# Kernel optimization log

Hardware: AMD Instinct MI355X
Metric: run time of the kernel (lower is better)

## Reference

```python
import jax, jax.numpy as jnp
import numpy as np

B, N, F, H, K, HID, TAB = 4, 256, 1024, 16, 128, 4096, 32
D = F // H
PI = 3.14159  # matches literal in source


def setup_inputs() -> dict:
    key = jax.random.key(0)
    ks = jax.random.split(key, 20)
    r = lambda i, shape: jax.random.normal(ks[i], shape, jnp.float32) * 0.02
    return dict(
        nfeat=jax.random.normal(ks[0], (B, N, F), jnp.float32),
        sp_dist=jax.random.randint(ks[1], (B, N, N), 0, TAB, dtype=jnp.int32),
        rd_dist=jax.random.uniform(ks[2], (B, N, N), jnp.float32),
        dist_table=r(3, (TAB, K)),
        g_means=jax.random.uniform(ks[4], (K,), jnp.float32, 0.0, 3.0),
        g_stds=jax.random.uniform(ks[5], (K,), jnp.float32, 0.0, 3.0),
        g_mul=jnp.ones((1,), jnp.float32),
        g_bias=jnp.zeros((1,), jnp.float32),
        mlp_w1=r(6, (2 * K, H)), mlp_b1=jnp.zeros((H,), jnp.float32),
        mlp_w2=r(7, (H, H)), mlp_b2=jnp.zeros((H,), jnp.float32),
        wq=r(8, (F, F)), bq=jnp.zeros((F,), jnp.float32),
        wk=r(9, (F, F)), bk=jnp.zeros((F,), jnp.float32),
        wv=r(10, (F, F)), bv=jnp.zeros((F,), jnp.float32),
        wo=r(11, (F, F)), bo=jnp.zeros((F,), jnp.float32),
        ffn_w1=r(12, (F, HID)), ffn_b1=jnp.zeros((HID,), jnp.float32),
        ffn_w2=r(13, (HID, F)), ffn_b2=jnp.zeros((F,), jnp.float32),
        ln1_g=jnp.ones((F,), jnp.float32), ln1_b=jnp.zeros((F,), jnp.float32),
        ln2_g=jnp.ones((F,), jnp.float32), ln2_b=jnp.zeros((F,), jnp.float32),
    )


def _layer_norm(x, g, b):
    m = x.mean(-1, keepdims=True)
    v = ((x - m) ** 2).mean(-1, keepdims=True)
    return (x - m) / jnp.sqrt(v + 1e-5) * g + b


def reference(nfeat, sp_dist, rd_dist, dist_table, g_means, g_stds, g_mul, g_bias,
              mlp_w1, mlp_b1, mlp_w2, mlp_b2, wq, bq, wk, bk, wv, bv, wo, bo,
              ffn_w1, ffn_b1, ffn_w2, ffn_b2, ln1_g, ln1_b, ln2_g, ln2_b):
    # --- FusedDistEncoder: shortest-path embedding + Gaussian resistance-distance encoding ---
    sp_emb = dist_table[sp_dist]                      # [B,N,N,K]
    x = g_mul * rd_dist[..., None] + g_bias           # [B,N,N,1] -> broadcast over K
    std = jnp.abs(g_stds) + 0.01                      # [K]
    rd_emb = jnp.exp(-0.5 * ((x - g_means) / std) ** 2) / (((2 * PI) ** 0.5) * std)
    h = jnp.concatenate([sp_emb, rd_emb], axis=-1)    # [B,N,N,2K]
    h = jax.nn.gelu(h @ mlp_w1 + mlp_b1, approximate=False)
    attn_bias = h @ mlp_w2 + mlp_b2                   # [B,N,N,H]

    # --- BiasedMultiheadAttention (note: source divides q by scaling=d^-0.5, i.e. *sqrt(d)) ---
    q = (nfeat @ wq + bq).reshape(B, N, H, D) * (D ** 0.5)
    k = (nfeat @ wk + bk).reshape(B, N, H, D)
    v = (nfeat @ wv + bv).reshape(B, N, H, D)
    scores = jnp.einsum('bihd,bjhd->bijh', q, k) + attn_bias   # [B,N,N,H]
    w = jax.nn.softmax(scores, axis=2)                          # softmax over key dim j
    attn = jnp.einsum('bijh,bjhd->bihd', w, v).reshape(B, N, F) @ wo + bo

    # --- GraphormerLayer residuals (post-norm, dropout=0 / eval) ---
    x1 = _layer_norm(nfeat + attn, ln1_g, ln1_b)
    ffn = jax.nn.relu(x1 @ ffn_w1 + ffn_b1) @ ffn_w2 + ffn_b2
    return _layer_norm(x1 + ffn, ln2_g, ln2_b)
```

## Files before the change

kernel.cpp:

```cpp
#include <hip/hip_runtime.h>
#include <hip/hip_bf16.h>
#include <math.h>

typedef __hip_bfloat16 bf16;
typedef float f32x4 __attribute__((ext_vector_type(4)));
typedef short bf16x8 __attribute__((ext_vector_type(8)));

#define AS1 __attribute__((address_space(1)))
#define AS3 __attribute__((address_space(3)))

#define ASM_VMCNT4 asm volatile("s_waitcnt vmcnt(4)" ::: "memory")
#define ASM_VMCNT0 asm volatile("s_waitcnt vmcnt(0)" ::: "memory")
#define ASM_LGKM0  asm volatile("s_waitcnt lgkmcnt(0)" ::: "memory")
#define ASM_BARRIER asm volatile("s_barrier" ::: "memory")

__global__ __launch_bounds__(256) void setup_kernel(
    const float* __restrict__ nfeat, bf16* __restrict__ nfeatb,
    const float* __restrict__ bq, const float* __restrict__ bk,
    const float* __restrict__ bv, float* __restrict__ bqkv,
    const float* __restrict__ table, const float* __restrict__ w1,
    float* __restrict__ tw)
{
    int bid = blockIdx.x, t = threadIdx.x;
    if (bid < 1024) {
        int i = (bid * 256 + t) * 4;
        float4 v = *reinterpret_cast<const float4*>(nfeat + i);
        nfeatb[i + 0] = (bf16)v.x; nfeatb[i + 1] = (bf16)v.y;
        nfeatb[i + 2] = (bf16)v.z; nfeatb[i + 3] = (bf16)v.w;
    } else if (bid < 1036) {
        int i = (bid - 1024) * 256 + t;
        bqkv[i] = i < 1024 ? bq[i] : (i < 2048 ? bk[i - 1024] : bv[i - 2048]);
    } else {
        #pragma unroll
        for (int e = t; e < 512; e += 256) {
            int r = e >> 4, o = e & 15;
            float a = 0.f;
            for (int k = 0; k < 128; ++k) a += table[r * 128 + k] * w1[k * 16 + o];
            tw[e] = a;
        }
    }
}

__global__ __launch_bounds__(256) void wtx_kernel(
    const float* __restrict__ wq, const float* __restrict__ wk,
    const float* __restrict__ wv, const float* __restrict__ wo,
    const float* __restrict__ fw1, const float* __restrict__ fw2,
    bf16* __restrict__ qkvT, bf16* __restrict__ woT,
    bf16* __restrict__ fw1T, bf16* __restrict__ fw2T)
{
    __shared__ float tile[64][68];
    int bid = blockIdx.x, t = threadIdx.x;
    const float* W; bf16* WT; int Kd, Nd, local;
    if (bid < 768)       { int ws = bid >> 8; local = bid & 255;
                           W = ws == 0 ? wq : ws == 1 ? wk : wv;
                           WT = qkvT + ws * 1048576; Kd = 1024; Nd = 1024; }
    else if (bid < 1024) { local = bid - 768;  W = wo;  WT = woT;  Kd = 1024; Nd = 1024; }
    else if (bid < 2048) { local = bid - 1024; W = fw1; WT = fw1T; Kd = 1024; Nd = 4096; }
    else                 { local = bid - 2048; W = fw2; WT = fw2T; Kd = 4096; Nd = 1024; }
    int ntn = Nd >> 6;
    int k0 = (local / ntn) * 64, n0 = (local % ntn) * 64;

    {
        int k = t >> 2, nb = (t & 3) * 16;
        const float* src = W + (size_t)(k0 + k) * Nd + n0 + nb;
        #pragma unroll
        for (int c = 0; c < 4; c++) {
            float4 v = *reinterpret_cast<const float4*>(src + c * 4);
            *reinterpret_cast<float4*>(&tile[k][nb + c * 4]) = v;
        }
    }
    __syncthreads();

    {
        int w = t >> 6, l = t & 63;
        int n = w * 16 + (l >> 2), kb = (l & 3) * 16;
        bf16x8 o0, o1;
        #pragma unroll
        for (int j = 0; j < 8; j++) {
            union { bf16 b; short s; } u;
            u.b = (bf16)tile[kb + j][n];
            o0[j] = u.s;
        }
        #pragma unroll
        for (int j = 0; j < 8; j++) {
            union { bf16 b; short s; } u;
            u.b = (bf16)tile[kb + 8 + j][n];
            o1[j] = u.s;
        }
        bf16* dst = WT + (size_t)(n0 + n) * Kd + k0 + kb;
        *reinterpret_cast<bf16x8*>(dst) = o0;
        *reinterpret_cast<bf16x8*>(dst + 8) = o1;
    }
}

__global__ __launch_bounds__(256) void enc_kernel(
    const int* __restrict__ sp, const float* __restrict__ rd,
    const float* __restrict__ tw,
    const float* __restrict__ means, const float* __restrict__ stds,
    const float* __restrict__ gmul, const float* __restrict__ gbias,
    const float* __restrict__ w1, const float* __restrict__ b1,
    const float* __restrict__ w2, const float* __restrict__ b2,
    bf16* __restrict__ biasT)
{
    __shared__ float w1s[128][16];
    __shared__ float w2s[16][16];
    __shared__ float b1s[16], b2s[16];
    __shared__ float meanS[128], istdS[128], coefS[128];
    int t = threadIdx.x;
    for (int i = t; i < 2048; i += 256) w1s[i >> 4][i & 15] = w1[2048 + i];
    w2s[t >> 4][t & 15] = w2[t];
    if (t < 16) { b1s[t] = b1[t]; b2s[t] = b2[t]; }
    if (t < 128) {
        float s = fabsf(stds[t]) + 0.01f;
        meanS[t] = means[t];
        istdS[t] = 1.f / s;
        coefS[t] = 1.f / (sqrtf(2.f * 3.14159f) * s);
    }
    __syncthreads();

    int p = blockIdx.x * 256 + t;
    int idx = sp[p];
    float xv = gmul[0] * rd[p] + gbias[0];

    float acc[16];
    #pragma unroll
    for (int o = 0; o < 16; o++) acc[o] = b1s[o] + tw[idx * 16 + o];

    for (int k = 0; k < 128; k++) {
        float d = (xv - meanS[k]) * istdS[k];
        float g = coefS[k] * __expf(-0.5f * d * d);
        #pragma unroll
        for (int o = 0; o < 16; o++) acc[o] += g * w1s[k][o];
    }
    float h[16];
    #pragma unroll
    for (int o = 0; o < 16; o++) {
        float a = acc[o];
        h[o] = 0.5f * a * (1.f + erff(a * 0.70710678118f));
    }
    float outv[16];
    #pragma unroll
    for (int o = 0; o < 16; o++) outv[o] = b2s[o];
    #pragma unroll
    for (int q = 0; q < 16; q++) {
        float hq = h[q];
        #pragma unroll
        for (int o = 0; o < 16; o++) outv[o] += hq * w2s[q][o];
    }
    int b = blockIdx.x >> 8, i = blockIdx.x & 255;
    #pragma unroll
    for (int hh = 0; hh < 16; hh++)
        biasT[(((b * 16 + hh) * 256 + i) << 8) + t] = (bf16)outv[hh];
}

__global__ __launch_bounds__(256, 4) void gemm_bf16(
    const bf16* __restrict__ A, const bf16* __restrict__ BT,
    const float* __restrict__ bias, const float* __restrict__ add,
    void* __restrict__ C, int M, int Nd, int Kd, int epi)
{
    __shared__ __align__(16) char smem[32768];
    int t = threadIdx.x;
    int w = t >> 6, l = t & 63;
    int wr = w >> 1, wc = w & 1;
    int lr = l & 15, hi = l >> 4;
    int row0 = blockIdx.y * 64, col0 = blockIdx.x * 64;
    int nz = gridDim.z;
    int klen = Kd / nz;
    int kbeg = blockIdx.z * klen;

    f32x4 acc[2][2];
    #pragma unroll
    for (int i = 0; i < 2; i++)
        #pragma unroll
        for (int j = 0; j < 2; j++) acc[i][j] = (f32x4){0.f, 0.f, 0.f, 0.f};

    const bf16* Asrc = A + (row0 + (t & 63)) * Kd + kbeg + (t >> 6) * 8;
    const bf16* Bsrc = BT + (col0 + (t & 63)) * Kd + kbeg + (t >> 6) * 8;
    int wbase = (t & 192) * 16;

    #pragma unroll
    for (int p = 0; p < 2; p++) {
        __builtin_amdgcn_global_load_lds((const AS1 void*)(Asrc + p * 32),
                                         (AS3 void*)(smem + p * 4096 + wbase), 16, 0, 0);
        __builtin_amdgcn_global_load_lds((const AS1 void*)(Bsrc + p * 32),
                                         (AS3 void*)(smem + 8192 + p * 4096 + wbase), 16, 0, 0);
    }

    int nsteps = klen >> 6;
    int cur = 0;
    for (int s = 0; s < nsteps; ++s) {
        int nxt = cur ^ 1;
        if (s + 1 < nsteps) {
            const bf16* An = Asrc + (s + 1) * 64;
            const bf16* Bn = Bsrc + (s + 1) * 64;
            #pragma unroll
            for (int p = 0; p < 2; p++) {
                __builtin_amdgcn_global_load_lds((const AS1 void*)(An + p * 32),
                    (AS3 void*)(smem + nxt * 16384 + p * 4096 + wbase), 16, 0, 0);
                __builtin_amdgcn_global_load_lds((const AS1 void*)(Bn + p * 32),
                    (AS3 void*)(smem + nxt * 16384 + 8192 + p * 4096 + wbase), 16, 0, 0);
            }
            ASM_VMCNT4;
        } else {
            ASM_VMCNT0;
        }
        ASM_BARRIER;

        const char* base = smem + cur * 16384;
        bf16x8 af[2][2], bfr[2][2];
        #pragma unroll
        for (int kk = 0; kk < 2; kk++) {
            #pragma unroll
            for (int mi = 0; mi < 2; mi++)
                af[kk][mi] = *(const bf16x8*)(base + kk * 4096 + hi * 1024 +
                                              (wr * 32 + mi * 16 + lr) * 16);
            #pragma unroll
            for (int nj = 0; nj < 2; nj++)
                bfr[kk][nj] = *(const bf16x8*)(base + 8192 + kk * 4096 + hi * 1024 +
                                               (wc * 32 + nj * 16 + lr) * 16);
        }
        ASM_LGKM0;
        __builtin_amdgcn_sched_barrier(0);
        ASM_BARRIER;
        __builtin_amdgcn_s_setprio(1);
        #pragma unroll
        for (int kk = 0; kk < 2; kk++)
            #pragma unroll
            for (int mi = 0; mi < 2; mi++)
                #pragma unroll
                for (int nj = 0; nj < 2; nj++)
                    acc[mi][nj] = __builtin_amdgcn_mfma_f32_16x16x32_bf16(
                        af[kk][mi], bfr[kk][nj], acc[mi][nj], 0, 0, 0);
        __builtin_amdgcn_s_setprio(0);
        cur = nxt;
    }

    if (nz > 1) {
        float* P = (float*)C + (size_t)blockIdx.z * M * Nd;
        #pragma unroll
        for (int i = 0; i < 2; i++) {
            int rb = row0 + wr * 32 + i * 16 + hi * 4;
            #pragma unroll
            for (int j = 0; j < 2; j++) {
                int cc = col0 + wc * 32 + j * 16 + lr;
                f32x4 v = acc[i][j];
                #pragma unroll
                for (int q = 0; q < 4; q++) P[(rb + q) * Nd + cc] = v[q];
            }
        }
        return;
    }

    #pragma unroll
    for (int i = 0; i < 2; i++) {
        int rb = row0 + wr * 32 + i * 16 + hi * 4;
        #pragma unroll
        for (int j = 0; j < 2; j++) {
            int cc = col0 + wc * 32 + j * 16 + lr;
            float bsv = bias[cc];
            f32x4 v = acc[i][j];
            #pragma unroll
            for (int q = 0; q < 4; q++) {
                int r = rb + q;
                float x = v[q] + bsv;
                if (epi == 0) {
                    ((float*)C)[r * Nd + cc] = x;
                } else if (epi == 1) {
                    ((float*)C)[r * Nd + cc] = x + add[r * Nd + cc];
                } else if (epi == 2) {
                    ((bf16*)C)[r * Nd + cc] = (bf16)fmaxf(x, 0.f);
                } else {
                    bf16* Cb = (bf16*)C;
                    int sel = cc >> 10, ccc = cc & 1023;
                    int hh = ccc >> 6, dd = ccc & 63;
                    int bb = r >> 8, ii = r & 255;
                    if (sel == 0)
                        Cb[(((bb * 16 + hh) * 256 + ii) << 6) + dd] = (bf16)(x * 8.0f);
                    else if (sel == 1)
                        Cb[1048576 + (((bb * 16 + hh) * 256 + ii) << 6) + dd] = (bf16)x;
                    else
                        Cb[2097152 + ((((bb * 16 + hh) << 6) + dd) << 8) + ii] = (bf16)x;
                }
            }
        }
    }
}

__global__ __launch_bounds__(256) void flash_kernel(
    const bf16* __restrict__ Qb, const bf16* __restrict__ Kb,
    const bf16* __restrict__ VT, const bf16* __restrict__ biasT,
    bf16* __restrict__ out)
{
    __shared__ __align__(16) char pls[32768];
    int t = threadIdx.x;
    int w = t >> 6, l = t & 63;
    int lr = l & 15, hi = l >> 4;
    int bh = blockIdx.x >> 2, iq = blockIdx.x & 3;
    int b = bh >> 4, h = bh & 15;
    int i0 = iq * 64 + w * 16;

    const bf16* Qp = Qb + (bh * 256 + i0 + lr) * 64 + hi * 8;
    bf16x8 qf0 = *(const bf16x8*)(Qp);
    bf16x8 qf1 = *(const bf16x8*)(Qp + 32);

    f32x4 acc[16];
    #pragma unroll
    for (int f = 0; f < 16; f++) acc[f] = (f32x4){0.f, 0.f, 0.f, 0.f};

    const bf16* Kp = Kb + (bh * 256 + lr) * 64 + hi * 8;
    #pragma unroll
    for (int f = 0; f < 16; f++) {
        bf16x8 kf0 = *(const bf16x8*)(Kp + f * 1024);
        bf16x8 kf1 = *(const bf16x8*)(Kp + f * 1024 + 32);
        acc[f] = __builtin_amdgcn_mfma_f32_16x16x32_bf16(qf0, kf0, acc[f], 0, 0, 0);
        acc[f] = __builtin_amdgcn_mfma_f32_16x16x32_bf16(qf1, kf1, acc[f], 0, 0, 0);
    }

    const bf16* bp = biasT + (bh * 256 + i0 + hi * 4) * 256 + lr;
    #pragma unroll
    for (int f = 0; f < 16; f++)
        #pragma unroll
        for (int q = 0; q < 4; q++)
            acc[f][q] += __bfloat162float(bp[q * 256 + f * 16]);

    float inv[4];
    #pragma unroll
    for (int q = 0; q < 4; q++) {
        float m = acc[0][q];
        #pragma unroll
        for (int f = 1; f < 16; f++) m = fmaxf(m, acc[f][q]);
        #pragma unroll
        for (int msk = 1; msk < 16; msk <<= 1) m = fmaxf(m, __shfl_xor(m, msk));
        float s = 0.f;
        #pragma unroll
        for (int f = 0; f < 16; f++) {
            float e = __expf(acc[f][q] - m);
            acc[f][q] = e;
            s += e;
        }
        #pragma unroll
        for (int msk = 1; msk < 16; msk <<= 1) s += __shfl_xor(s, msk);
        inv[q] = 1.f / s;
    }

    char* Pw = pls + w * 8192;
    #pragma unroll
    for (int f = 0; f < 16; f++) {
        int j = f * 16 + lr;
        int c = j >> 3, jo = j & 7;
        #pragma unroll
        for (int q = 0; q < 4; q++)
            *(bf16*)(Pw + c * 256 + (hi * 4 + q) * 16 + jo * 2) = (bf16)(acc[f][q] * inv[q]);
    }
    __syncthreads();

    const char* Pr = pls + w * 8192 + hi * 256 + lr * 16;
    const bf16* Vp = VT + (bh * 64 + lr) * 256 + hi * 8;
    #pragma unroll
    for (int n = 0; n < 4; n++) {
        f32x4 o = (f32x4){0.f, 0.f, 0.f, 0.f};
        #pragma unroll
        for (int ks = 0; ks < 8; ks++) {
            bf16x8 pa = *(const bf16x8*)(Pr + ks * 1024);
            bf16x8 vb = *(const bf16x8*)(Vp + n * 4096 + ks * 32);
            o = __builtin_amdgcn_mfma_f32_16x16x32_bf16(pa, vb, o, 0, 0, 0);
        }
        #pragma unroll
        for (int q = 0; q < 4; q++)
            out[(b * 256 + i0 + hi * 4 + q) * 1024 + h * 64 + n * 16 + lr] = (bf16)o[q];
    }
}

__global__ __launch_bounds__(256) void ln_fused_kernel(
    const float* __restrict__ part, int S,
    const float* __restrict__ bias, const float* __restrict__ add,
    const float* __restrict__ g, const float* __restrict__ bta,
    float* __restrict__ out, bf16* __restrict__ ob)
{
    int row = blockIdx.x;
    int t = threadIdx.x;
    float v[4];
    float sum = 0.f;
    #pragma unroll
    for (int i = 0; i < 4; i++) {
        int c = t + i * 256;
        float x = add[row * 1024 + c] + bias[c];
        for (int s = 0; s < S; s++) x += part[s * 1048576 + row * 1024 + c];
        v[i] = x;
        sum += x;
    }
    __shared__ float red[8];
    #pragma unroll
    for (int off = 32; off; off >>= 1) sum += __shfl_xor(sum, off);
    if ((t & 63) == 0) red[t >> 6] = sum;
    __syncthreads();
    float mean = (red[0] + red[1] + red[2] + red[3]) * (1.f / 1024.f);
    float vs = 0.f;
    #pragma unroll
    for (int i = 0; i < 4; i++) { float d = v[i] - mean; vs += d * d; }
    #pragma unroll
    for (int off = 32; off; off >>= 1) vs += __shfl_xor(vs, off);
    if ((t & 63) == 0) red[4 + (t >> 6)] = vs;
    __syncthreads();
    float var = (red[4] + red[5] + red[6] + red[7]) * (1.f / 1024.f);
    float invs = rsqrtf(var + 1e-5f);
    #pragma unroll
    for (int i = 0; i < 4; i++) {
        int c = t + i * 256;
        float o = (v[i] - mean) * invs * g[c] + bta[c];
        out[row * 1024 + c] = o;
        if (ob) ob[row * 1024 + c] = (bf16)o;
    }
}

extern "C" void kernel_launch(void* const* d_in, const int* in_sizes, int n_in,
                              void* d_out, int out_size, void* d_ws, size_t ws_size,
                              hipStream_t stream)
{
    const float* nfeat  = (const float*)d_in[0];
    const int*   sp     = (const int*)  d_in[1];
    const float* rd     = (const float*)d_in[2];
    const float* table  = (const float*)d_in[3];
    const float* gmeans = (const float*)d_in[4];
    const float* gstds  = (const float*)d_in[5];
    const float* gmul   = (const float*)d_in[6];
    const float* gbias  = (const float*)d_in[7];
    const float* w1     = (const float*)d_in[8];
    const float* b1     = (const float*)d_in[9];
    const float* w2     = (const float*)d_in[10];
    const float* b2     = (const float*)d_in[11];
    const float* wq     = (const float*)d_in[12];
    const float* bq     = (const float*)d_in[13];
    const float* wk     = (const float*)d_in[14];
    const float* bk     = (const float*)d_in[15];
    const float* wv     = (const float*)d_in[16];
    const float* bv     = (const float*)d_in[17];
    const float* wo     = (const float*)d_in[18];
    const float* bo     = (const float*)d_in[19];
    const float* fw1    = (const float*)d_in[20];
    const float* fb1    = (const float*)d_in[21];
    const float* fw2    = (const float*)d_in[22];
    const float* fb2    = (const float*)d_in[23];
    const float* ln1g   = (const float*)d_in[24];
    const float* ln1b   = (const float*)d_in[25];
    const float* ln2g   = (const float*)d_in[26];
    const float* ln2b   = (const float*)d_in[27];

    const size_t MB = 1 << 20;
    char* cws = (char*)d_ws;
    bf16*  biasT   = (bf16*)(cws);
    bf16*  qkvb    = (bf16*)(cws + 8 * MB);
    float* part    = (float*)(cws + 8 * MB);
    bf16*  qkvT    = (bf16*)(cws + 16 * MB);
    bf16*  woT     = (bf16*)(cws + 22 * MB);
    bf16*  fw1T    = (bf16*)(cws + 24 * MB);
    bf16*  fw2T    = (bf16*)(cws + 32 * MB);
    float* x1      = (float*)(cws + 40 * MB);
    bf16*  nfeatb  = (bf16*)(cws + 44 * MB);
    bf16*  x1b     = (bf16*)(cws + 46 * MB);
    bf16*  attnob  = (bf16*)(cws + 48 * MB);
    float* bqkv    = (float*)(cws + 50 * MB);
    float* tw      = (float*)(cws + 50 * MB + 16384);
    bf16*  hiddenb = biasT;

    setup_kernel<<<1037, 256, 0, stream>>>(nfeat, nfeatb, bq, bk, bv, bqkv,
                                           table, w1, tw);
    wtx_kernel<<<3072, 256, 0, stream>>>(wq, wk, wv, wo, fw1, fw2,
                                         qkvT, woT, fw1T, fw2T);
    enc_kernel<<<1024, 256, 0, stream>>>(sp, rd, tw, gmeans, gstds, gmul, gbias,
                                         w1, b1, w2, b2, biasT);

    gemm_bf16<<<dim3(48, 16), 256, 0, stream>>>(nfeatb, qkvT, bqkv, nullptr, qkvb,
                                                1024, 3072, 1024, 3);

    flash_kernel<<<256, 256, 0, stream>>>(qkvb, qkvb + 1048576, qkvb + 2097152,
                                          biasT, attnob);

    gemm_bf16<<<dim3(16, 16, 2), 256, 0, stream>>>(attnob, woT, bo, nullptr, part,
                                                   1024, 1024, 1024, 0);
    ln_fused_kernel<<<1024, 256, 0, stream>>>(part, 2, bo, nfeat, ln1g, ln1b, x1, x1b);

    gemm_bf16<<<dim3(64, 16), 256, 0, stream>>>(x1b, fw1T, fb1, nullptr, hiddenb,
                                                1024, 4096, 1024, 2);

    gemm_bf16<<<dim3(16, 16, 4), 256, 0, stream>>>(hiddenb, fw2T, fb2, nullptr, part,
                                                   1024, 1024, 4096, 0);
    ln_fused_kernel<<<1024, 256, 0, stream>>>(part, 4, fb2, x1, ln2g, ln2b,
                                              (float*)d_out, nullptr);
}
```

Measured before the change: 193.3 us.

## Enlarge GEMM tiles to 128x128 and split-K the QKV projection

The GEMM kernel moves from 64x64 to 128x128 output tiles with a 4x4 MFMA accumulator per wave and a K-step of 32. The hand-written waitcnt/barrier/setprio scheduling is replaced by plain __syncthreads, and occupancy is lowered to 2 blocks per CU. The QKV projection now uses split-K into fp32 partials, followed by a separate combine kernel that adds bias and scatters the head-major Q/K/V layouts. The output projection uses split-K 4, and the workspace is re-laid out to hold the larger partial buffer. Larger tiles improve operand reuse, but they produce far fewer blocks, which may underfill the GPU, and the extra partial write and combine pass add memory traffic.

```diff
diff --git a/kernel.cpp b/kernel.cpp
--- a/kernel.cpp
+++ b/kernel.cpp
@@ -8,11 +8,6 @@
 
 #define AS1 __attribute__((address_space(1)))
 #define AS3 __attribute__((address_space(3)))
-
-#define ASM_VMCNT4 asm volatile("s_waitcnt vmcnt(4)" ::: "memory")
-#define ASM_VMCNT0 asm volatile("s_waitcnt vmcnt(0)" ::: "memory")
-#define ASM_LGKM0  asm volatile("s_waitcnt lgkmcnt(0)" ::: "memory")
-#define ASM_BARRIER asm volatile("s_barrier" ::: "memory")
 
 __global__ __launch_bounds__(256) void setup_kernel(
     const float* __restrict__ nfeat, bf16* __restrict__ nfeatb,
@@ -153,136 +148,132 @@
         biasT[(((b * 16 + hh) * 256 + i) << 8) + t] = (bf16)outv[hh];
 }
 
-__global__ __launch_bounds__(256, 4) void gemm_bf16(
+__global__ __launch_bounds__(256, 2) void gemm_bf16(
     const bf16* __restrict__ A, const bf16* __restrict__ BT,
-    const float* __restrict__ bias, const float* __restrict__ add,
-    void* __restrict__ C, int M, int Nd, int Kd, int epi)
+    const float* __restrict__ bias, void* __restrict__ C,
+    int M, int Nd, int Kd, int epi)
 {
     __shared__ __align__(16) char smem[32768];
     int t = threadIdx.x;
     int w = t >> 6, l = t & 63;
     int wr = w >> 1, wc = w & 1;
-    int lr = l & 15, hi = l >> 4;
-    int row0 = blockIdx.y * 64, col0 = blockIdx.x * 64;
+    int lr = l & 15, lc = l >> 4;
+    int row0 = blockIdx.y * 128, col0 = blockIdx.x * 128;
     int nz = gridDim.z;
-    int klen = Kd / nz;
-    int kbeg = blockIdx.z * klen;
-
-    f32x4 acc[2][2];
-    #pragma unroll
-    for (int i = 0; i < 2; i++)
-        #pragma unroll
-        for (int j = 0; j < 2; j++) acc[i][j] = (f32x4){0.f, 0.f, 0.f, 0.f};
-
-    const bf16* Asrc = A + (row0 + (t & 63)) * Kd + kbeg + (t >> 6) * 8;
-    const bf16* Bsrc = BT + (col0 + (t & 63)) * Kd + kbeg + (t >> 6) * 8;
+    int klen = Kd / nz, kbeg = blockIdx.z * klen;
+
+    f32x4 acc[4][4];
+    #pragma unroll
+    for (int i = 0; i < 4; i++)
+        #pragma unroll
+        for (int j = 0; j < 4; j++) acc[i][j] = (f32x4){0.f, 0.f, 0.f, 0.f};
+
+    int sr = t & 127, sc = t >> 7;
+    const bf16* Asrc = A + (size_t)(row0 + sr) * Kd + kbeg + sc * 8;
+    const bf16* Bsrc = BT + (size_t)(col0 + sr) * Kd + kbeg + sc * 8;
     int wbase = (t & 192) * 16;
 
+    int aoff = lc * 2048 + (wr * 64 + lr) * 16;
+    int boff = 8192 + lc * 2048 + (wc * 64 + lr) * 16;
+
     #pragma unroll
     for (int p = 0; p < 2; p++) {
-        __builtin_amdgcn_global_load_lds((const AS1 void*)(Asrc + p * 32),
-                                         (AS3 void*)(smem + p * 4096 + wbase), 16, 0, 0);
-        __builtin_amdgcn_global_load_lds((const AS1 void*)(Bsrc + p * 32),
-                                         (AS3 void*)(smem + 8192 + p * 4096 + wbase), 16, 0, 0);
-    }
-
-    int nsteps = klen >> 6;
-    int cur = 0;
+        __builtin_amdgcn_global_load_lds((const AS1 void*)(Asrc + p * 16),
+            (AS3 void*)(smem + p * 4096 + wbase), 16, 0, 0);
+        __builtin_amdgcn_global_load_lds((const AS1 void*)(Bsrc + p * 16),
+            (AS3 void*)(smem + 8192 + p * 4096 + wbase), 16, 0, 0);
+    }
+    __syncthreads();
+
+    int nsteps = klen >> 5;
     for (int s = 0; s < nsteps; ++s) {
-        int nxt = cur ^ 1;
+        int cur = s & 1;
         if (s + 1 < nsteps) {
-            const bf16* An = Asrc + (s + 1) * 64;
-            const bf16* Bn = Bsrc + (s + 1) * 64;
+            const bf16* An = Asrc + (s + 1) * 32;
+            const bf16* Bn = Bsrc + (s + 1) * 32;
+            char* dst = smem + (cur ^ 1) * 16384;
             #pragma unroll
             for (int p = 0; p < 2; p++) {
-                __builtin_amdgcn_global_load_lds((const AS1 void*)(An + p * 32),
-                    (AS3 void*)(smem + nxt * 16384 + p * 4096 + wbase), 16, 0, 0);
-                __builtin_amdgcn_global_load_lds((const AS1 void*)(Bn + p * 32),
-                    (AS3 void*)(smem + nxt * 16384 + 8192 + p * 4096 + wbase), 16, 0, 0);
+                __builtin_amdgcn_global_load_lds((const AS1 void*)(An + p * 16),
+                    (AS3 void*)(dst + p * 4096 + wbase), 16, 0, 0);
+                __builtin_amdgcn_global_load_lds((const AS1 void*)(Bn + p * 16),
+                    (AS3 void*)(dst + 8192 + p * 4096 + wbase), 16, 0, 0);
             }
-            ASM_VMCNT4;
-        } else {
-            ASM_VMCNT0;
-        }
-        ASM_BARRIER;
-
+        }
         const char* base = smem + cur * 16384;
-        bf16x8 af[2][2], bfr[2][2];
-        #pragma unroll
-        for (int kk = 0; kk < 2; kk++) {
+        bf16x8 af[4], bfr[4];
+        #pragma unroll
+        for (int i = 0; i < 4; i++) af[i] = *(const bf16x8*)(base + aoff + i * 256);
+        #pragma unroll
+        for (int j = 0; j < 4; j++) bfr[j] = *(const bf16x8*)(base + boff + j * 256);
+        #pragma unroll
+        for (int i = 0; i < 4; i++)
             #pragma unroll
-            for (int mi = 0; mi < 2; mi++)
-                af[kk][mi] = *(const bf16x8*)(base + kk * 4096 + hi * 1024 +
-                                              (wr * 32 + mi * 16 + lr) * 16);
-            #pragma unroll
-            for (int nj = 0; nj < 2; nj++)
-                bfr[kk][nj] = *(const bf16x8*)(base + 8192 + kk * 4096 + hi * 1024 +
-                                               (wc * 32 + nj * 16 + lr) * 16);
-        }
-        ASM_LGKM0;
-        __builtin_amdgcn_sched_barrier(0);
-        ASM_BARRIER;
-        __builtin_amdgcn_s_setprio(1);
-        #pragma unroll
-        for (int kk = 0; kk < 2; kk++)
-            #pragma unroll
-            for (int mi = 0; mi < 2; mi++)
-                #pragma unroll
-                for (int nj = 0; nj < 2; nj++)
-                    acc[mi][nj] = __builtin_amdgcn_mfma_f32_16x16x32_bf16(
-                        af[kk][mi], bfr[kk][nj], acc[mi][nj], 0, 0, 0);
-        __builtin_amdgcn_s_setprio(0);
-        cur = nxt;
+            for (int j = 0; j < 4; j++)
+                acc[i][j] = __builtin_amdgcn_mfma_f32_16x16x32_bf16(
+                    af[i], bfr[j], acc[i][j], 0, 0, 0);
+        __syncthreads();
     }
 
     if (nz > 1) {
         float* P = (float*)C + (size_t)blockIdx.z * M * Nd;
         #pragma unroll
-        for (int i = 0; i < 2; i++) {
-            int rb = row0 + wr * 32 + i * 16 + hi * 4;
+        for (int i = 0; i < 4; i++) {
+            int rb = row0 + wr * 64 + i * 16 + lc * 4;
             #pragma unroll
-            for (int j = 0; j < 2; j++) {
-                int cc = col0 + wc * 32 + j * 16 + lr;
+            for (int j = 0; j < 4; j++) {
+                int cc = col0 + wc * 64 + j * 16 + lr;
                 f32x4 v = acc[i][j];
                 #pragma unroll
-                for (int q = 0; q < 4; q++) P[(rb + q) * Nd + cc] = v[q];
+                for (int q = 0; q < 4; q++) P[(size_t)(rb + q) * Nd + cc] = v[q];
             }
         }
         return;
     }
 
     #pragma unroll
-    for (int i = 0; i < 2; i++) {
-        int rb = row0 + wr * 32 + i * 16 + hi * 4;
-        #pragma unroll
-        for (int j = 0; j < 2; j++) {
-            int cc = col0 + wc * 32 + j * 16 + lr;
+    for (int i = 0; i < 4; i++) {
+        int rb = row0 + wr * 64 + i * 16 + lc * 4;
+        #pragma unroll
+        for (int j = 0; j < 4; j++) {
+            int cc = col0 + wc * 64 + j * 16 + lr;
             float bsv = bias[cc];
             f32x4 v = acc[i][j];
             #pragma unroll
             for (int q = 0; q < 4; q++) {
                 int r = rb + q;
                 float x = v[q] + bsv;
-                if (epi == 0) {
-                    ((float*)C)[r * Nd + cc] = x;
-                } else if (epi == 1) {
-                    ((float*)C)[r * Nd + cc] = x + add[r * Nd + cc];
-                } else if (epi == 2) {
-                    ((bf16*)C)[r * Nd + cc] = (bf16)fmaxf(x, 0.f);
-                } else {
-                    bf16* Cb = (bf16*)C;
-                    int sel = cc >> 10, ccc = cc & 1023;
-                    int hh = ccc >> 6, dd = ccc & 63;
-                    int bb = r >> 8, ii = r & 255;
-                    if (sel == 0)
-                        Cb[(((bb * 16 + hh) * 256 + ii) << 6) + dd] = (bf16)(x * 8.0f);
-                    else if (sel == 1)
-                        Cb[1048576 + (((bb * 16 + hh) * 256 + ii) << 6) + dd] = (bf16)x;
-                    else
-                        Cb[2097152 + ((((bb * 16 + hh) << 6) + dd) << 8) + ii] = (bf16)x;
-                }
+                if (epi == 2) ((bf16*)C)[(size_t)r * Nd + cc] = (bf16)fmaxf(x, 0.f);
+                else          ((float*)C)[(size_t)r * Nd + cc] = x;
             }
         }
+    }
+}
+
+__global__ __launch_bounds__(256) void qkv_combine_kernel(
+    const float* __restrict__ part, const float* __restrict__ bqkv,
+    bf16* __restrict__ qkvb)
+{
+    int e0 = (blockIdx.x * 256 + threadIdx.x) * 4;
+    int r = e0 / 3072, cc0 = e0 - r * 3072;
+    float4 p0 = *(const float4*)(part + e0);
+    float4 p1 = *(const float4*)(part + 3145728 + e0);
+    float4 bs = *(const float4*)(bqkv + cc0);
+    float x[4] = {p0.x + p1.x + bs.x, p0.y + p1.y + bs.y,
+                  p0.z + p1.z + bs.z, p0.w + p1.w + bs.w};
+    int bb = r >> 8, ii = r & 255;
+    int sel = cc0 >> 10, ccc0 = cc0 & 1023;
+    int hh = ccc0 >> 6, dd0 = ccc0 & 63;
+    #pragma unroll
+    for (int u = 0; u < 4; u++) {
+        float v = x[u];
+        int dd = dd0 + u;
+        if (sel == 0)
+            qkvb[(((bb * 16 + hh) * 256 + ii) << 6) + dd] = (bf16)(v * 8.0f);
+        else if (sel == 1)
+            qkvb[1048576 + (((bb * 16 + hh) * 256 + ii) << 6) + dd] = (bf16)v;
+        else
+            qkvb[2097152 + ((((bb * 16 + hh) << 6) + dd) << 8) + ii] = (bf16)v;
     }
 }
 
@@ -450,17 +441,17 @@
     char* cws = (char*)d_ws;
     bf16*  biasT   = (bf16*)(cws);
     bf16*  qkvb    = (bf16*)(cws + 8 * MB);
-    float* part    = (float*)(cws + 8 * MB);
-    bf16*  qkvT    = (bf16*)(cws + 16 * MB);
-    bf16*  woT     = (bf16*)(cws + 22 * MB);
-    bf16*  fw1T    = (bf16*)(cws + 24 * MB);
-    bf16*  fw2T    = (bf16*)(cws + 32 * MB);
-    float* x1      = (float*)(cws + 40 * MB);
-    bf16*  nfeatb  = (bf16*)(cws + 44 * MB);
-    bf16*  x1b     = (bf16*)(cws + 46 * MB);
-    bf16*  attnob  = (bf16*)(cws + 48 * MB);
-    float* bqkv    = (float*)(cws + 50 * MB);
-    float* tw      = (float*)(cws + 50 * MB + 16384);
+    float* part    = (float*)(cws + 16 * MB);
+    bf16*  qkvT    = (bf16*)(cws + 48 * MB);
+    bf16*  woT     = (bf16*)(cws + 54 * MB);
+    bf16*  fw1T    = (bf16*)(cws + 56 * MB);
+    bf16*  fw2T    = (bf16*)(cws + 64 * MB);
+    float* x1      = (float*)(cws + 72 * MB);
+    bf16*  nfeatb  = (bf16*)(cws + 76 * MB);
+    bf16*  x1b     = (bf16*)(cws + 78 * MB);
+    bf16*  attnob  = (bf16*)(cws + 80 * MB);
+    float* bqkv    = (float*)(cws + 82 * MB);
+    float* tw      = (float*)(cws + 82 * MB + 16384);
     bf16*  hiddenb = biasT;
 
     setup_kernel<<<1037, 256, 0, stream>>>(nfeat, nfeatb, bq, bk, bv, bqkv,
@@ -470,21 +461,22 @@
     enc_kernel<<<1024, 256, 0, stream>>>(sp, rd, tw, gmeans, gstds, gmul, gbias,
                                          w1, b1, w2, b2, biasT);
 
-    gemm_bf16<<<dim3(48, 16), 256, 0, stream>>>(nfeatb, qkvT, bqkv, nullptr, qkvb,
-                                                1024, 3072, 1024, 3);
+    gemm_bf16<<<dim3(24, 8, 2), 256, 0, stream>>>(nfeatb, qkvT, nullptr, part,
+                                                  1024, 3072, 1024, 0);
+    qkv_combine_kernel<<<3072, 256, 0, stream>>>(part, bqkv, qkvb);
 
     flash_kernel<<<256, 256, 0, stream>>>(qkvb, qkvb + 1048576, qkvb + 2097152,
                                           biasT, attnob);
 
-    gemm_bf16<<<dim3(16, 16, 2), 256, 0, stream>>>(attnob, woT, bo, nullptr, part,
-                                                   1024, 1024, 1024, 0);
-    ln_fused_kernel<<<1024, 256, 0, stream>>>(part, 2, bo, nfeat, ln1g, ln1b, x1, x1b);
-
-    gemm_bf16<<<dim3(64, 16), 256, 0, stream>>>(x1b, fw1T, fb1, nullptr, hiddenb,
-                                                1024, 4096, 1024, 2);
-
-    gemm_bf16<<<dim3(16, 16, 4), 256, 0, stream>>>(hiddenb, fw2T, fb2, nullptr, part,
-                                                   1024, 1024, 4096, 0);
+    gemm_bf16<<<dim3(8, 8, 4), 256, 0, stream>>>(attnob, woT, nullptr, part,
+                                                 1024, 1024, 1024, 0);
+    ln_fused_kernel<<<1024, 256, 0, stream>>>(part, 4, bo, nfeat, ln1g, ln1b, x1, x1b);
+
+    gemm_bf16<<<dim3(32, 8), 256, 0, stream>>>(x1b, fw1T, fb1, hiddenb,
+                                               1024, 4096, 1024, 2);
+
+    gemm_bf16<<<dim3(8, 8, 4), 256, 0, stream>>>(hiddenb, fw2T, nullptr, part,
+                                                 1024, 1024, 4096, 0);
     ln_fused_kernel<<<1024, 256, 0, stream>>>(part, 4, fb2, x1, ln2g, ln2b,
                                               (float*)d_out, nullptr);
 }
```

Result: no change. 196.0 us (+1.4%).
